# Performance work log

Measured on AMD Instinct MI355X. Metric: run time of the kernel, lower is better.

Reference implementation:

```python
import jax, jax.numpy as jnp
import numpy as np
import math

D_MODEL = 64
H = 8
DK = D_MODEL // H


def setup_inputs() -> dict:
    key = jax.random.key(0)
    ks = jax.random.split(key, 6)
    B, C, T, N = 8, D_MODEL, 12, 307
    x = jax.random.normal(ks[0], (B, C, T, N), dtype=jnp.float32)
    mask = jax.random.randint(ks[1], (B, N, N), 0, 2, dtype=jnp.int32)
    s = 1.0 / math.sqrt(D_MODEL)
    Wq = jax.random.uniform(ks[2], (D_MODEL, D_MODEL), jnp.float32, -s, s)
    bq = jax.random.uniform(ks[3], (D_MODEL,), jnp.float32, -s, s)
    Wk = jax.random.uniform(ks[4], (D_MODEL, D_MODEL), jnp.float32, -s, s)
    bk = jax.random.uniform(ks[5], (D_MODEL,), jnp.float32, -s, s)
    return {"x": x, "mask": mask, "Wq": Wq, "bq": bq, "Wk": Wk, "bk": bk}


def reference(x, mask, Wq, bq, Wk, bk):
    # x: [B, d_model, T, N] -> [B, T, N, d_model]
    B, C, T, N = x.shape
    xp = jnp.transpose(x, (0, 2, 3, 1))
    # torch Linear: y = x W^T + b
    q = jnp.einsum('btnd,ed->btne', xp, Wq) + bq
    k = jnp.einsum('btnd,ed->btne', xp, Wk) + bk
    # split heads: [B, T, N, h, dk]
    q = q.reshape(B, T, N, H, DK)
    k = k.reshape(B, T, N, H, DK)
    # QK^T per head then sum over heads (einsum 'ijkmn->ijmn'), fused:
    # scores: [B, T, N, N]
    scores = jnp.einsum('btnhd,btmhd->btnm', q, k) / math.sqrt(DK)
    # mask.unsqueeze(1) -> [B, 1, N, N]
    scores = jnp.where(mask[:, None] == 0, jnp.float32(-1e9), scores)
    # softmax over last dim; dropout is identity in eval mode
    return jax.nn.softmax(scores, axis=-1)
```

## Files before the change

kernel.cpp:

```cpp
#include <hip/hip_runtime.h>
#include <math.h>

#define PB 8
#define PT 12
#define PN 307
#define NP 320
#define SCALE 0.35355339059327373f

typedef short bf16x8 __attribute__((ext_vector_type(8)));
typedef float f32x4  __attribute__((ext_vector_type(4)));

__device__ __forceinline__ unsigned short f32_to_bf16(float v) {
    unsigned u = __float_as_uint(v);
    u += 0x7FFFu + ((u >> 16) & 1u);
    return (unsigned short)(u >> 16);
}

__global__ __launch_bounds__(256) void qk_proj_kernel(
    const float* __restrict__ x,
    const float* __restrict__ Wq, const float* __restrict__ bq,
    const float* __restrict__ Wk, const float* __restrict__ bk,
    unsigned short* __restrict__ qws, unsigned short* __restrict__ kws)
{
    __shared__ float wqT[64 * 65];
    __shared__ float wkT[64 * 65];
    __shared__ float xs[64][36];

    const int tid = threadIdx.x;
    const int chunk = blockIdx.x % 10;
    const int bt = blockIdx.x / 10;
    const int b = bt / PT, t = bt % PT;
    const int n0 = chunk * 32;

    for (int idx = tid; idx < 4096; idx += 256) {
        int e = idx >> 6, c = idx & 63;
        wqT[c * 65 + e] = Wq[idx];
        wkT[c * 65 + e] = Wk[idx];
    }
    for (int idx = tid; idx < 2048; idx += 256) {
        int c = idx >> 5, nl = idx & 31;
        int n = n0 + nl;
        xs[c][nl] = (n < PN) ? x[((b * 64 + c) * PT + t) * PN + n] : 0.f;
    }
    __syncthreads();

    const int e  = tid & 63;
    const int rg = (tid >> 6) * 8;

    float accq[8], acck[8];
    const float bqv = bq[e], bkv = bk[e];
    #pragma unroll
    for (int j = 0; j < 8; ++j) { accq[j] = bqv; acck[j] = bkv; }

    #pragma unroll 4
    for (int c = 0; c < 64; ++c) {
        const float wq = wqT[c * 65 + e];
        const float wk = wkT[c * 65 + e];
        const float4 x0 = *(const float4*)&xs[c][rg];
        const float4 x1 = *(const float4*)&xs[c][rg + 4];
        accq[0] = fmaf(x0.x, wq, accq[0]);  acck[0] = fmaf(x0.x, wk, acck[0]);
        accq[1] = fmaf(x0.y, wq, accq[1]);  acck[1] = fmaf(x0.y, wk, acck[1]);
        accq[2] = fmaf(x0.z, wq, accq[2]);  acck[2] = fmaf(x0.z, wk, acck[2]);
        accq[3] = fmaf(x0.w, wq, accq[3]);  acck[3] = fmaf(x0.w, wk, acck[3]);
        accq[4] = fmaf(x1.x, wq, accq[4]);  acck[4] = fmaf(x1.x, wk, acck[4]);
        accq[5] = fmaf(x1.y, wq, accq[5]);  acck[5] = fmaf(x1.y, wk, acck[5]);
        accq[6] = fmaf(x1.z, wq, accq[6]);  acck[6] = fmaf(x1.z, wk, acck[6]);
        accq[7] = fmaf(x1.w, wq, accq[7]);  acck[7] = fmaf(x1.w, wk, acck[7]);
    }

    #pragma unroll
    for (int j = 0; j < 8; ++j) {
        const int n = n0 + rg + j;
        const bool v = (n < PN);
        qws[((size_t)bt * NP + n) * 64 + e] = v ? f32_to_bf16(accq[j]) : (unsigned short)0;
        kws[((size_t)bt * NP + n) * 64 + e] = v ? f32_to_bf16(acck[j]) : (unsigned short)0;
    }
}

__global__ __launch_bounds__(256) void attn_kernel(
    const unsigned short* __restrict__ qws,
    const unsigned short* __restrict__ kws,
    const int* __restrict__ mask,
    float* __restrict__ out)
{
    const int tid  = threadIdx.x;
    const int lane = tid & 63;
    const int wv   = tid >> 6;
    const int chunk = blockIdx.x % 5;
    const int bt    = blockIdx.x / 5;
    const int b     = bt / PT;
    const int n0    = chunk * 64 + wv * 16;
    const int rlo   = lane & 15;
    const int kq    = lane >> 4;

    f32x4 acc[20] = {};

    const bf16x8* qp = (const bf16x8*)(qws + ((size_t)bt * NP + n0 + rlo) * 64 + kq * 8);
    const unsigned short* kbase0 = kws + ((size_t)bt * NP + rlo) * 64 + kq * 8;

    #pragma unroll
    for (int ks = 0; ks < 2; ++ks) {
        const bf16x8 afr = qp[ks * 4];
        const unsigned short* kb = kbase0 + ks * 32;
        #pragma unroll
        for (int ct = 0; ct < 20; ++ct) {
            const bf16x8 bfr = *(const bf16x8*)(kb + (size_t)ct * 16 * 64);
            acc[ct] = __builtin_amdgcn_mfma_f32_16x16x32_bf16(afr, bfr, acc[ct], 0, 0, 0);
        }
    }

    float mx[4] = {-INFINITY, -INFINITY, -INFINITY, -INFINITY};
    #pragma unroll
    for (int ct = 0; ct < 20; ++ct) {
        const int m = ct * 16 + rlo;
        const bool mval = (m < PN);
        #pragma unroll
        for (int r = 0; r < 4; ++r) {
            const int n  = n0 + kq * 4 + r;
            const int nn = (n < PN) ? n : (PN - 1);
            float s;
            if (mval) {
                const int mk = mask[((size_t)b * PN + nn) * PN + m];
                s = mk ? acc[ct][r] * SCALE : -1e9f;
            } else {
                s = -INFINITY;
            }
            acc[ct][r] = s;
            mx[r] = fmaxf(mx[r], s);
        }
    }
    #pragma unroll
    for (int off = 1; off <= 8; off <<= 1) {
        #pragma unroll
        for (int r = 0; r < 4; ++r) mx[r] = fmaxf(mx[r], __shfl_xor(mx[r], off));
    }

    float sum[4] = {0.f, 0.f, 0.f, 0.f};
    #pragma unroll
    for (int ct = 0; ct < 20; ++ct) {
        #pragma unroll
        for (int r = 0; r < 4; ++r) {
            const float p = __expf(acc[ct][r] - mx[r]);
            acc[ct][r] = p;
            sum[r] += p;
        }
    }
    #pragma unroll
    for (int off = 1; off <= 8; off <<= 1) {
        #pragma unroll
        for (int r = 0; r < 4; ++r) sum[r] += __shfl_xor(sum[r], off);
    }
    float inv[4];
    #pragma unroll
    for (int r = 0; r < 4; ++r) inv[r] = 1.0f / sum[r];

    #pragma unroll
    for (int ct = 0; ct < 20; ++ct) {
        const int m = ct * 16 + rlo;
        if (m < PN) {
            #pragma unroll
            for (int r = 0; r < 4; ++r) {
                const int n = n0 + kq * 4 + r;
                if (n < PN)
                    out[((size_t)bt * PN + n) * PN + m] = acc[ct][r] * inv[r];
            }
        }
    }
}

extern "C" void kernel_launch(void* const* d_in, const int* in_sizes, int n_in,
                              void* d_out, int out_size, void* d_ws, size_t ws_size,
                              hipStream_t stream) {
    const float* x  = (const float*)d_in[0];
    const int* mask = (const int*)d_in[1];
    const float* Wq = (const float*)d_in[2];
    const float* bq = (const float*)d_in[3];
    const float* Wk = (const float*)d_in[4];
    const float* bk = (const float*)d_in[5];
    float* out = (float*)d_out;

    unsigned short* qws = (unsigned short*)d_ws;
    unsigned short* kws = qws + (size_t)96 * NP * 64;

    qk_proj_kernel<<<dim3(96 * 10), dim3(256), 0, stream>>>(x, Wq, bq, Wk, bk, qws, kws);
    attn_kernel<<<dim3(96 * 5), dim3(256), 0, stream>>>(qws, kws, mask, out);
}
```

Measured before the change: 112.4 us.

## Use MFMA for QK projection and transpose attention tiles for vectorized mask/output access

The Q/K projection kernel drops its LDS-staged scalar FMA loop. It now converts x and the weights to bf16 in registers and computes with 16x16x32 bf16 MFMA, launching 128-thread blocks. In the attention kernel the MFMA operands are swapped so each lane owns one query row. That lets the mask be read and the output written as 4-wide vectors, and cuts the row-reduction shuffles to two steps. In exchange the projection rounds its inputs to bf16, which adds error, and padded workspace rows are no longer zeroed. The mask read also slightly overruns row ends, which is harmless except at the very end of the buffer.

```diff
diff --git a/kernel.cpp b/kernel.cpp
--- a/kernel.cpp
+++ b/kernel.cpp
@@ -9,6 +9,8 @@
 
 typedef short bf16x8 __attribute__((ext_vector_type(8)));
 typedef float f32x4  __attribute__((ext_vector_type(4)));
+typedef int   i32x4u __attribute__((ext_vector_type(4), aligned(4)));
+typedef float f32x4u __attribute__((ext_vector_type(4), aligned(4)));
 
 __device__ __forceinline__ unsigned short f32_to_bf16(float v) {
     unsigned u = __float_as_uint(v);
@@ -16,64 +18,71 @@
     return (unsigned short)(u >> 16);
 }
 
-__global__ __launch_bounds__(256) void qk_proj_kernel(
+__device__ __forceinline__ bf16x8 pack8(float4 lo, float4 hi) {
+    bf16x8 r;
+    r[0] = (short)f32_to_bf16(lo.x); r[1] = (short)f32_to_bf16(lo.y);
+    r[2] = (short)f32_to_bf16(lo.z); r[3] = (short)f32_to_bf16(lo.w);
+    r[4] = (short)f32_to_bf16(hi.x); r[5] = (short)f32_to_bf16(hi.y);
+    r[6] = (short)f32_to_bf16(hi.z); r[7] = (short)f32_to_bf16(hi.w);
+    return r;
+}
+
+__global__ __launch_bounds__(128) void qk_proj_kernel(
     const float* __restrict__ x,
     const float* __restrict__ Wq, const float* __restrict__ bq,
     const float* __restrict__ Wk, const float* __restrict__ bk,
     unsigned short* __restrict__ qws, unsigned short* __restrict__ kws)
 {
-    __shared__ float wqT[64 * 65];
-    __shared__ float wkT[64 * 65];
-    __shared__ float xs[64][36];
+    const int tid  = threadIdx.x;
+    const int lane = tid & 63;
+    const int wv   = tid >> 6;
+    const int chunk = blockIdx.x % 10;
+    const int bt    = blockIdx.x / 10;
+    const int b = bt / PT, t = bt % PT;
+    const int rlo = lane & 15;
+    const int kq  = lane >> 4;
+    const int n0  = chunk * 32 + wv * 16;
 
-    const int tid = threadIdx.x;
-    const int chunk = blockIdx.x % 10;
-    const int bt = blockIdx.x / 10;
-    const int b = bt / PT, t = bt % PT;
-    const int n0 = chunk * 32;
+    const int nn = min(n0 + rlo, PN - 1);
+    const float* xrow = x + ((size_t)b * 64 * PT + t) * PN + nn;
+    bf16x8 a[2];
+    #pragma unroll
+    for (int ks = 0; ks < 2; ++ks) {
+        #pragma unroll
+        for (int j = 0; j < 8; ++j) {
+            const int c = ks * 32 + kq * 8 + j;
+            a[ks][j] = (short)f32_to_bf16(xrow[(size_t)c * PT * PN]);
+        }
+    }
 
-    for (int idx = tid; idx < 4096; idx += 256) {
-        int e = idx >> 6, c = idx & 63;
-        wqT[c * 65 + e] = Wq[idx];
-        wkT[c * 65 + e] = Wk[idx];
-    }
-    for (int idx = tid; idx < 2048; idx += 256) {
-        int c = idx >> 5, nl = idx & 31;
-        int n = n0 + nl;
-        xs[c][nl] = (n < PN) ? x[((b * 64 + c) * PT + t) * PN + n] : 0.f;
-    }
-    __syncthreads();
-
-    const int e  = tid & 63;
-    const int rg = (tid >> 6) * 8;
-
-    float accq[8], acck[8];
-    const float bqv = bq[e], bkv = bk[e];
+    f32x4 accq[4] = {}, acck[4] = {};
     #pragma unroll
-    for (int j = 0; j < 8; ++j) { accq[j] = bqv; acck[j] = bkv; }
-
-    #pragma unroll 4
-    for (int c = 0; c < 64; ++c) {
-        const float wq = wqT[c * 65 + e];
-        const float wk = wkT[c * 65 + e];
-        const float4 x0 = *(const float4*)&xs[c][rg];
-        const float4 x1 = *(const float4*)&xs[c][rg + 4];
-        accq[0] = fmaf(x0.x, wq, accq[0]);  acck[0] = fmaf(x0.x, wk, acck[0]);
-        accq[1] = fmaf(x0.y, wq, accq[1]);  acck[1] = fmaf(x0.y, wk, acck[1]);
-        accq[2] = fmaf(x0.z, wq, accq[2]);  acck[2] = fmaf(x0.z, wk, acck[2]);
-        accq[3] = fmaf(x0.w, wq, accq[3]);  acck[3] = fmaf(x0.w, wk, acck[3]);
-        accq[4] = fmaf(x1.x, wq, accq[4]);  acck[4] = fmaf(x1.x, wk, acck[4]);
-        accq[5] = fmaf(x1.y, wq, accq[5]);  acck[5] = fmaf(x1.y, wk, acck[5]);
-        accq[6] = fmaf(x1.z, wq, accq[6]);  acck[6] = fmaf(x1.z, wk, acck[6]);
-        accq[7] = fmaf(x1.w, wq, accq[7]);  acck[7] = fmaf(x1.w, wk, acck[7]);
+    for (int et = 0; et < 4; ++et) {
+        const float* wq_r = Wq + (size_t)(et * 16 + rlo) * 64 + kq * 8;
+        const float* wk_r = Wk + (size_t)(et * 16 + rlo) * 64 + kq * 8;
+        #pragma unroll
+        for (int ks = 0; ks < 2; ++ks) {
+            const bf16x8 bqf = pack8(*(const float4*)(wq_r + ks * 32),
+                                     *(const float4*)(wq_r + ks * 32 + 4));
+            const bf16x8 bkf = pack8(*(const float4*)(wk_r + ks * 32),
+                                     *(const float4*)(wk_r + ks * 32 + 4));
+            accq[et] = __builtin_amdgcn_mfma_f32_16x16x32_bf16(a[ks], bqf, accq[et], 0, 0, 0);
+            acck[et] = __builtin_amdgcn_mfma_f32_16x16x32_bf16(a[ks], bkf, acck[et], 0, 0, 0);
+        }
     }
 
     #pragma unroll
-    for (int j = 0; j < 8; ++j) {
-        const int n = n0 + rg + j;
-        const bool v = (n < PN);
-        qws[((size_t)bt * NP + n) * 64 + e] = v ? f32_to_bf16(accq[j]) : (unsigned short)0;
-        kws[((size_t)bt * NP + n) * 64 + e] = v ? f32_to_bf16(acck[j]) : (unsigned short)0;
+    for (int et = 0; et < 4; ++et) {
+        const int e = et * 16 + rlo;
+        const float bqv = bq[e], bkv = bk[e];
+        #pragma unroll
+        for (int r = 0; r < 4; ++r) {
+            const int n = n0 + kq * 4 + r;
+            if (n < PN) {
+                qws[((size_t)bt * NP + n) * 64 + e] = f32_to_bf16(accq[et][r] + bqv);
+                kws[((size_t)bt * NP + n) * 64 + e] = f32_to_bf16(acck[et][r] + bkv);
+            }
+        }
     }
 }
 
@@ -89,82 +98,77 @@
     const int chunk = blockIdx.x % 5;
     const int bt    = blockIdx.x / 5;
     const int b     = bt / PT;
-    const int n0    = chunk * 64 + wv * 16;
-    const int rlo   = lane & 15;
-    const int kq    = lane >> 4;
+    const int ng  = chunk * 64 + wv * 16;
+    const int nl  = lane & 15;
+    const int kq  = lane >> 4;
+    const int n   = ng + nl;
+    const int nn  = (n < PN) ? n : (PN - 1);
+
+    const bf16x8* qp = (const bf16x8*)(qws + ((size_t)bt * NP + n) * 64 + kq * 8);
+    const unsigned short* kbase = kws + ((size_t)bt * NP + nl) * 64 + kq * 8;
 
     f32x4 acc[20] = {};
-
-    const bf16x8* qp = (const bf16x8*)(qws + ((size_t)bt * NP + n0 + rlo) * 64 + kq * 8);
-    const unsigned short* kbase0 = kws + ((size_t)bt * NP + rlo) * 64 + kq * 8;
-
     #pragma unroll
     for (int ks = 0; ks < 2; ++ks) {
-        const bf16x8 afr = qp[ks * 4];
-        const unsigned short* kb = kbase0 + ks * 32;
+        const bf16x8 bqf = qp[ks * 4];
+        const unsigned short* kb = kbase + ks * 32;
         #pragma unroll
         for (int ct = 0; ct < 20; ++ct) {
-            const bf16x8 bfr = *(const bf16x8*)(kb + (size_t)ct * 16 * 64);
-            acc[ct] = __builtin_amdgcn_mfma_f32_16x16x32_bf16(afr, bfr, acc[ct], 0, 0, 0);
+            const bf16x8 af = *(const bf16x8*)(kb + (size_t)ct * 16 * 64);
+            acc[ct] = __builtin_amdgcn_mfma_f32_16x16x32_bf16(af, bqf, acc[ct], 0, 0, 0);
         }
     }
 
-    float mx[4] = {-INFINITY, -INFINITY, -INFINITY, -INFINITY};
+    const int* mrow = mask + ((size_t)b * PN + nn) * PN;
+    float mx = -INFINITY;
     #pragma unroll
     for (int ct = 0; ct < 20; ++ct) {
-        const int m = ct * 16 + rlo;
-        const bool mval = (m < PN);
+        const int m0 = ct * 16 + kq * 4;
+        const i32x4u mv = *(const i32x4u*)(mrow + m0);
+        float sv[4];
+        sv[0] = mv[0] ? acc[ct][0] * SCALE : -1e9f;
+        sv[1] = mv[1] ? acc[ct][1] * SCALE : -1e9f;
+        sv[2] = mv[2] ? acc[ct][2] * SCALE : -1e9f;
+        sv[3] = mv[3] ? acc[ct][3] * SCALE : -1e9f;
+        if (ct == 19) {
+            #pragma unroll
+            for (int r = 0; r < 4; ++r)
+                if (m0 + r >= PN) sv[r] = -INFINITY;
+        }
         #pragma unroll
-        for (int r = 0; r < 4; ++r) {
-            const int n  = n0 + kq * 4 + r;
-            const int nn = (n < PN) ? n : (PN - 1);
-            float s;
-            if (mval) {
-                const int mk = mask[((size_t)b * PN + nn) * PN + m];
-                s = mk ? acc[ct][r] * SCALE : -1e9f;
-            } else {
-                s = -INFINITY;
-            }
-            acc[ct][r] = s;
-            mx[r] = fmaxf(mx[r], s);
-        }
+        for (int r = 0; r < 4; ++r) { acc[ct][r] = sv[r]; mx = fmaxf(mx, sv[r]); }
     }
-    #pragma unroll
-    for (int off = 1; off <= 8; off <<= 1) {
-        #pragma unroll
-        for (int r = 0; r < 4; ++r) mx[r] = fmaxf(mx[r], __shfl_xor(mx[r], off));
-    }
+    mx = fmaxf(mx, __shfl_xor(mx, 16));
+    mx = fmaxf(mx, __shfl_xor(mx, 32));
 
-    float sum[4] = {0.f, 0.f, 0.f, 0.f};
+    float sum = 0.f;
     #pragma unroll
     for (int ct = 0; ct < 20; ++ct) {
         #pragma unroll
         for (int r = 0; r < 4; ++r) {
-            const float p = __expf(acc[ct][r] - mx[r]);
+            const float p = __expf(acc[ct][r] - mx);
             acc[ct][r] = p;
-            sum[r] += p;
+            sum += p;
         }
     }
-    #pragma unroll
-    for (int off = 1; off <= 8; off <<= 1) {
+    sum += __shfl_xor(sum, 16);
+    sum += __shfl_xor(sum, 32);
+    const float inv = 1.0f / sum;
+
+    if (n < PN) {
+        float* orow = out + ((size_t)bt * PN + n) * PN;
         #pragma unroll
-        for (int r = 0; r < 4; ++r) sum[r] += __shfl_xor(sum[r], off);
-    }
-    float inv[4];
-    #pragma unroll
-    for (int r = 0; r < 4; ++r) inv[r] = 1.0f / sum[r];
-
-    #pragma unroll
-    for (int ct = 0; ct < 20; ++ct) {
-        const int m = ct * 16 + rlo;
-        if (m < PN) {
-            #pragma unroll
-            for (int r = 0; r < 4; ++r) {
-                const int n = n0 + kq * 4 + r;
-                if (n < PN)
-                    out[((size_t)bt * PN + n) * PN + m] = acc[ct][r] * inv[r];
-            }
+        for (int ct = 0; ct < 19; ++ct) {
+            const int m0 = ct * 16 + kq * 4;
+            f32x4u o;
+            o[0] = acc[ct][0] * inv; o[1] = acc[ct][1] * inv;
+            o[2] = acc[ct][2] * inv; o[3] = acc[ct][3] * inv;
+            *(f32x4u*)(orow + m0) = o;
         }
+        const int m0 = 304 + kq * 4;
+        #pragma unroll
+        for (int r = 0; r < 4; ++r)
+            if (m0 + r < PN) orow[m0 + r] = acc[19][r] * inv;
     }
 }
 
@@ -182,6 +186,6 @@
     unsigned short* qws = (unsigned short*)d_ws;
     unsigned short* kws = qws + (size_t)96 * NP * 64;
 
-    qk_proj_kernel<<<dim3(96 * 10), dim3(256), 0, stream>>>(x, Wq, bq, Wk, bk, qws, kws);
+    qk_proj_kernel<<<dim3(96 * 10), dim3(128), 0, stream>>>(x, Wq, bq, Wk, bk, qws, kws);
     attn_kernel<<<dim3(96 * 5), dim3(256), 0, stream>>>(qws, kws, mask, out);
 }
```

Measured after the change: 108.8 us. 1.03x faster.
